# Kernel optimization log

Measured on AMD Instinct MI355X. Metric: run time of the kernel, lower is better.

## Reference

```python
import jax, jax.numpy as jnp
import numpy as np

N_NODES = 100000
N_EDGES = 1600000
DIM = 64          # num_features == hidden_dim
N_LAYERS = 5
N_GRAPHS = 1024
EMB = DIM * N_LAYERS  # 320
BN_EPS = 1e-5


def setup_inputs() -> dict:
    key = jax.random.key(0)
    ks = jax.random.split(key, 16)
    s = 0.05
    return {
        "x": jax.random.normal(ks[0], (N_NODES, DIM), dtype=jnp.float32),
        "edge_index": jax.random.randint(ks[1], (2, N_EDGES), 0, N_NODES, dtype=jnp.int32),
        "edge_weight": jax.random.uniform(ks[2], (N_EDGES,), dtype=jnp.float32),
        "batch": jnp.sort(jax.random.randint(ks[3], (N_NODES,), 0, N_GRAPHS, dtype=jnp.int32)),
        # stacked per-layer GIN MLP params: nn = Linear(d,d) -> ReLU -> Linear(d,d)
        "W1s": jax.random.normal(ks[4], (N_LAYERS, DIM, DIM), dtype=jnp.float32) * s,
        "b1s": jnp.zeros((N_LAYERS, DIM), dtype=jnp.float32),
        "W2s": jax.random.normal(ks[5], (N_LAYERS, DIM, DIM), dtype=jnp.float32) * s,
        "b2s": jnp.zeros((N_LAYERS, DIM), dtype=jnp.float32),
        # BatchNorm1d affine params (init: weight=1, bias=0)
        "gammas": jnp.ones((N_LAYERS, DIM), dtype=jnp.float32),
        "betas": jnp.zeros((N_LAYERS, DIM), dtype=jnp.float32),
        # projection head: Linear(EMB,EMB) -> ReLU -> Linear(EMB,EMB)
        "pW1": jax.random.normal(ks[6], (EMB, EMB), dtype=jnp.float32) * s,
        "pb1": jnp.zeros((EMB,), dtype=jnp.float32),
        "pW2": jax.random.normal(ks[7], (EMB, EMB), dtype=jnp.float32) * s,
        "pb2": jnp.zeros((EMB,), dtype=jnp.float32),
    }


def _encoder(x, src, dst, edge_weight, batch,
             W1s, b1s, W2s, b2s, gammas, betas):
    h = x
    pooled = []
    for i in range(N_LAYERS):
        # WGINConv (eps=0): h_out = nn(h + sum_{j->i} w_ij * h_j)
        msg = jax.ops.segment_sum(h[src] * edge_weight[:, None], dst,
                                  num_segments=N_NODES)  # [N, D]
        z = h + msg
        z = jnp.maximum(z @ W1s[i] + b1s[i], 0.0) @ W2s[i] + b2s[i]
        h = jnp.maximum(z, 0.0)  # F.relu after conv
        # BatchNorm1d (training mode: batch stats over nodes, biased var)
        mean = jnp.mean(h, axis=0)
        var = jnp.var(h, axis=0)
        h = (h - mean) * jax.lax.rsqrt(var + BN_EPS) * gammas[i] + betas[i]
        pooled.append(h)
    # global_mean_pool per layer, then concat along feature dim
    counts = jax.ops.segment_sum(jnp.ones((N_NODES,), h.dtype), batch,
                                 num_segments=N_GRAPHS)
    counts = jnp.maximum(counts, 1.0)[:, None]
    xpool = [jax.ops.segment_sum(h, batch, num_segments=N_GRAPHS) / counts
             for h in pooled]
    return jnp.concatenate(xpool, axis=1)  # [G, L*D]


def reference(x, edge_index, edge_weight, batch,
              W1s, b1s, W2s, b2s, gammas, betas,
              pW1, pb1, pW2, pb2):
    src, dst = edge_index[0], edge_index[1]
    y = _encoder(x, src, dst, edge_weight, batch,
                 W1s, b1s, W2s, b2s, gammas, betas)
    # proj_head: Linear -> ReLU -> Linear
    y = jnp.maximum(y @ pW1 + pb1, 0.0) @ pW2 + pb2
    return y
```

## Files before the change

### kernel.cpp

```cpp
#include <hip/hip_runtime.h>

#define NN 100000
#define NE 1600000
#define D 64
#define NL 5
#define NG 1024
#define EMBD 320
#define BN_EPS 1e-5f
#define SCAN_NB ((NN + 255) / 256)
#define GIN_NB ((NN + 63) / 64)
#define SRCB 7
#define M2 (NN * SRCB)
#define SCAN2_NB ((M2 + 255) / 256)

__device__ __forceinline__ unsigned short bf16rne(float f) {
  unsigned u = __float_as_uint(f);
  unsigned r = u + 0x7FFFu + ((u >> 16) & 1u);
  return (unsigned short)(r >> 16);
}
__device__ __forceinline__ float bflo(int v) {
  return __uint_as_float(((unsigned)v) << 16);
}
__device__ __forceinline__ float bfhi(int v) {
  return __uint_as_float(((unsigned)v) & 0xFFFF0000u);
}

__global__ __launch_bounds__(256) void k_cvt(const float* __restrict__ in,
                                             unsigned short* __restrict__ outb) {
  int i = blockIdx.x * 256 + threadIdx.x;
  if (i >= NN * 16) return;
  float4 v = ((const float4*)in)[i];
  ushort4 o;
  o.x = bf16rne(v.x); o.y = bf16rne(v.y); o.z = bf16rne(v.z); o.w = bf16rne(v.w);
  ((ushort4*)outb)[i] = o;
}

__global__ __launch_bounds__(256) void k_gbound(const int* __restrict__ batch,
                                                int* __restrict__ gstart) {
  int i = blockIdx.x * 256 + threadIdx.x;
  if (i >= NN) return;
  int b = batch[i];
  int bp = (i == 0) ? -1 : batch[i - 1];
  for (int g = bp + 1; g <= b; ++g) gstart[g] = i;
  if (i == NN - 1) {
    for (int g = b + 1; g <= NG; ++g) gstart[g] = NN;
  }
}

__global__ __launch_bounds__(256) void k_hist(const int* __restrict__ src,
                                              const int* __restrict__ dst,
                                              int* __restrict__ deg) {
  int e = blockIdx.x * 256 + threadIdx.x;
  if (e >= NE) return;
  int s = __builtin_nontemporal_load(src + e);
  int d = __builtin_nontemporal_load(dst + e);
  atomicAdd(&deg[d * SRCB + (s >> 14)], 1);
}

__global__ __launch_bounds__(256) void k_scan1(const int* __restrict__ deg,
                                               int* __restrict__ bsums) {
  __shared__ int sh[256];
  int i = blockIdx.x * 256 + threadIdx.x;
  sh[threadIdx.x] = (i < M2) ? deg[i] : 0;
  __syncthreads();
  for (int off = 128; off > 0; off >>= 1) {
    if (threadIdx.x < off) sh[threadIdx.x] += sh[threadIdx.x + off];
    __syncthreads();
  }
  if (threadIdx.x == 0) bsums[blockIdx.x] = sh[0];
}

__global__ __launch_bounds__(1024) void k_scan2(int* __restrict__ bsums) {
  __shared__ int sh[1024];
  int t = threadIdx.x;
  int loc[3];
  int s = 0;
#pragma unroll
  for (int i = 0; i < 3; ++i) {
    int idx = t * 3 + i;
    loc[i] = s;
    if (idx < SCAN2_NB) s += bsums[idx];
  }
  sh[t] = s;
  __syncthreads();
  for (int off = 1; off < 1024; off <<= 1) {
    int u = (t >= off) ? sh[t - off] : 0;
    __syncthreads();
    sh[t] += u;
    __syncthreads();
  }
  int base = sh[t] - s;
#pragma unroll
  for (int i = 0; i < 3; ++i) {
    int idx = t * 3 + i;
    if (idx < SCAN2_NB) bsums[idx] = base + loc[i];
  }
}

__global__ __launch_bounds__(256) void k_scan3(int* __restrict__ row_ptr,
                                               int* __restrict__ cursor,
                                               const int* __restrict__ bsums) {
  __shared__ int sh[256];
  int t = threadIdx.x;
  int i = blockIdx.x * 256 + t;
  int v = (i < M2) ? row_ptr[i] : 0;
  sh[t] = v;
  __syncthreads();
  for (int off = 1; off < 256; off <<= 1) {
    int u = (t >= off) ? sh[t - off] : 0;
    __syncthreads();
    sh[t] += u;
    __syncthreads();
  }
  int excl = sh[t] - v + bsums[blockIdx.x];
  if (i < M2) {
    row_ptr[i] = excl;
    cursor[i] = excl;
    if (i == M2 - 1) row_ptr[M2] = excl + v;
  }
}

__global__ __launch_bounds__(256) void k_fill(const int* __restrict__ src,
                                              const int* __restrict__ dst,
                                              const float* __restrict__ w,
                                              int* __restrict__ cursor,
                                              int2* __restrict__ epair) {
  int e = blockIdx.x * 256 + threadIdx.x;
  if (e >= NE) return;
  int s = __builtin_nontemporal_load(src + e);
  int d = __builtin_nontemporal_load(dst + e);
  float we = __builtin_nontemporal_load(w + e);
  int slot = atomicAdd(&cursor[d * SRCB + (s >> 14)], 1);
  int2 p;
  p.x = s;
  p.y = __float_as_int(we);
  epair[slot] = p;
}

#define ACC8(CA, CB, WE)                                                      \
  a0.x = fmaf(bflo(CA.x), WE, a0.x); a0.y = fmaf(bfhi(CA.x), WE, a0.y);       \
  a0.z = fmaf(bflo(CA.y), WE, a0.z); a0.w = fmaf(bfhi(CA.y), WE, a0.w);       \
  a1.x = fmaf(bflo(CA.z), WE, a1.x); a1.y = fmaf(bfhi(CA.z), WE, a1.y);       \
  a1.z = fmaf(bflo(CA.w), WE, a1.z); a1.w = fmaf(bfhi(CA.w), WE, a1.w);       \
  a2.x = fmaf(bflo(CB.x), WE, a2.x); a2.y = fmaf(bfhi(CB.x), WE, a2.y);       \
  a2.z = fmaf(bflo(CB.y), WE, a2.z); a2.w = fmaf(bfhi(CB.y), WE, a2.w);       \
  a3.x = fmaf(bflo(CB.z), WE, a3.x); a3.y = fmaf(bfhi(CB.z), WE, a3.y);       \
  a3.z = fmaf(bflo(CB.w), WE, a3.z); a3.w = fmaf(bfhi(CB.w), WE, a3.w);

__global__ __launch_bounds__(256, 6) void k_gin(const float* __restrict__ x0,
                                                const unsigned short* __restrict__ hbf,
                                                unsigned short* __restrict__ gbf,
                                                const int* __restrict__ row_ptr,
                                                const int2* __restrict__ epair,
                                                const float* __restrict__ W1,
                                                const float* __restrict__ b1,
                                                const float* __restrict__ W2,
                                                const float* __restrict__ b2,
                                                const float* __restrict__ statsP,
                                                const float* __restrict__ gammaP,
                                                const float* __restrict__ betaP,
                                                int first,
                                                float* __restrict__ statsL) {
  __shared__ float zin[64 * 65];
  __shared__ float sW[32 * 64];
  __shared__ float sb[64];
  __shared__ float wsumS[64];
  __shared__ float scA[64], sbA[64];
  const int t = threadIdx.x;
  const int nb = blockIdx.x * 64;
  const int nr = t >> 4, fc = t & 15;

  for (int i = t; i < 2048; i += 256) sW[i] = W1[i];
  if (t < 64) {
    sb[t] = b1[t];
    if (!first) {
      float m = statsP[t] * (1.f / NN);
      float v = fmaxf(statsP[64 + t] * (1.f / NN) - m * m, 0.f);
      float sc = gammaP[t] * rsqrtf(v + BN_EPS);
      scA[t] = sc;
      sbA[t] = betaP[t] - m * sc;
    }
  }

  {
    const int nl = t >> 2;
    const int q = t & 3;
    const int n = nb + nl;
    float4 a0 = {0.f, 0.f, 0.f, 0.f}, a1 = a0, a2 = a0, a3 = a0;
    float wsum = 0.f;
    if (n < NN) {
      const int beg = row_ptr[n * SRCB], end = row_ptr[n * SRCB + SRCB];
      int i = beg;
      for (; i + 2 <= end; i += 2) {
        long long e0 = __builtin_nontemporal_load((const long long*)(epair + i));
        long long e1 = __builtin_nontemporal_load((const long long*)(epair + i + 1));
        int s0 = (int)(e0 & 0xFFFFFFFFll);
        float w0 = __int_as_float((int)(e0 >> 32));
        int s1 = (int)(e1 & 0xFFFFFFFFll);
        float w1 = __int_as_float((int)(e1 >> 32));
        const int4* p0 = (const int4*)(hbf + (size_t)s0 * D);
        const int4* p1 = (const int4*)(hbf + (size_t)s1 * D);
        int4 r0a = p0[2 * q], r0b = p0[2 * q + 1];
        int4 r1a = p1[2 * q], r1b = p1[2 * q + 1];
        ACC8(r0a, r0b, w0)
        wsum += w0;
        ACC8(r1a, r1b, w1)
        wsum += w1;
      }
      for (; i < end; ++i) {
        long long e0 = __builtin_nontemporal_load((const long long*)(epair + i));
        int s0 = (int)(e0 & 0xFFFFFFFFll);
        float w0 = __int_as_float((int)(e0 >> 32));
        const int4* p0 = (const int4*)(hbf + (size_t)s0 * D);
        int4 r0a = p0[2 * q], r0b = p0[2 * q + 1];
        ACC8(r0a, r0b, w0)
        wsum += w0;
      }
      if (first) {
        const float4* own = (const float4*)(x0 + (size_t)n * D) + q * 4;
        float4 o0 = own[0], o1 = own[1], o2 = own[2], o3 = own[3];
        a0.x += o0.x; a0.y += o0.y; a0.z += o0.z; a0.w += o0.w;
        a1.x += o1.x; a1.y += o1.y; a1.z += o1.z; a1.w += o1.w;
        a2.x += o2.x; a2.y += o2.y; a2.z += o2.z; a2.w += o2.w;
        a3.x += o3.x; a3.y += o3.y; a3.z += o3.z; a3.w += o3.w;
      } else {
        const int4* hp = (const int4*)(hbf + (size_t)n * D);
        int4 c0 = hp[2 * q], c1 = hp[2 * q + 1];
        a0.x += bflo(c0.x); a0.y += bfhi(c0.x);
        a0.z += bflo(c0.y); a0.w += bfhi(c0.y);
        a1.x += bflo(c0.z); a1.y += bfhi(c0.z);
        a1.z += bflo(c0.w); a1.w += bfhi(c0.w);
        a2.x += bflo(c1.x); a2.y += bfhi(c1.x);
        a2.z += bflo(c1.y); a2.w += bfhi(c1.y);
        a3.x += bflo(c1.z); a3.y += bfhi(c1.z);
        a3.z += bflo(c1.w); a3.w += bfhi(c1.w);
      }
    }
    float* zr = &zin[nl * 65 + q * 16];
    *(float4*)(zr + 0) = a0;
    *(float4*)(zr + 4) = a1;
    *(float4*)(zr + 8) = a2;
    *(float4*)(zr + 12) = a3;
    if (q == 0) wsumS[nl] = wsum;
  }
  __syncthreads();

  if (!first) {
#pragma unroll
    for (int pass = 0; pass < 4; ++pass) {
      int idx = pass * 1024 + t * 4;
      int r = idx >> 6, c = idx & 63;
      float wp1 = 1.f + wsumS[r];
      float4 z = *(float4*)&zin[r * 65 + c];
      z.x = fmaf(z.x, scA[c + 0], sbA[c + 0] * wp1);
      z.y = fmaf(z.y, scA[c + 1], sbA[c + 1] * wp1);
      z.z = fmaf(z.z, scA[c + 2], sbA[c + 2] * wp1);
      z.w = fmaf(z.w, scA[c + 3], sbA[c + 3] * wp1);
      *(float4*)&zin[r * 65 + c] = z;
    }
    __syncthreads();
  }

#define GEMM_HALF(ACC, KBASE)                                                 \
  _Pragma("unroll 2") for (int kc = 0; kc < 8; ++kc) {                        \
    float4 zv[4], wv[4];                                                      \
    _Pragma("unroll") for (int i = 0; i < 4; ++i)                             \
        zv[i] = *(float4*)&zin[(nr * 4 + i) * 65 + ((KBASE) + kc) * 4];       \
    _Pragma("unroll") for (int kk = 0; kk < 4; ++kk)                          \
        wv[kk] = *(float4*)&sW[(kc * 4 + kk) * 64 + fc * 4];                  \
    _Pragma("unroll") for (int i = 0; i < 4; ++i) {                           \
      ACC[i].x = fmaf(zv[i].x, wv[0].x, ACC[i].x);                            \
      ACC[i].y = fmaf(zv[i].x, wv[0].y, ACC[i].y);                            \
      ACC[i].z = fmaf(zv[i].x, wv[0].z, ACC[i].z);                            \
      ACC[i].w = fmaf(zv[i].x, wv[0].w, ACC[i].w);                            \
      ACC[i].x = fmaf(zv[i].y, wv[1].x, ACC[i].x);                            \
      ACC[i].y = fmaf(zv[i].y, wv[1].y, ACC[i].y);                            \
      ACC[i].z = fmaf(zv[i].y, wv[1].z, ACC[i].z);                            \
      ACC[i].w = fmaf(zv[i].y, wv[1].w, ACC[i].w);                            \
      ACC[i].x = fmaf(zv[i].z, wv[2].x, ACC[i].x);                            \
      ACC[i].y = fmaf(zv[i].z, wv[2].y, ACC[i].y);                            \
      ACC[i].z = fmaf(zv[i].z, wv[2].z, ACC[i].z);                            \
      ACC[i].w = fmaf(zv[i].z, wv[2].w, ACC[i].w);                            \
      ACC[i].x = fmaf(zv[i].w, wv[3].x, ACC[i].x);                            \
      ACC[i].y = fmaf(zv[i].w, wv[3].y, ACC[i].y);                            \
      ACC[i].z = fmaf(zv[i].w, wv[3].z, ACC[i].z);                            \
      ACC[i].w = fmaf(zv[i].w, wv[3].w, ACC[i].w);                            \
    }                                                                         \
  }

#define RELU4(ACC)                                                            \
  _Pragma("unroll") for (int i = 0; i < 4; ++i) {                             \
    ACC[i].x = fmaxf(ACC[i].x, 0.f);                                          \
    ACC[i].y = fmaxf(ACC[i].y, 0.f);                                          \
    ACC[i].z = fmaxf(ACC[i].z, 0.f);                                          \
    ACC[i].w = fmaxf(ACC[i].w, 0.f);                                          \
  }

  float4 acc[4];
  {
    float4 bias = *(float4*)&sb[fc * 4];
#pragma unroll
    for (int i = 0; i < 4; ++i) acc[i] = bias;
  }
  GEMM_HALF(acc, 0)
  __syncthreads();
  for (int i = t; i < 2048; i += 256) sW[i] = W1[2048 + i];
  __syncthreads();
  GEMM_HALF(acc, 8)
  RELU4(acc)
  __syncthreads();

#pragma unroll
  for (int i = 0; i < 4; ++i) *(float4*)&zin[(nr * 4 + i) * 65 + fc * 4] = acc[i];
  for (int i = t; i < 2048; i += 256) sW[i] = W2[i];
  if (t < 64) sb[t] = b2[t];
  __syncthreads();

  float4 acc2[4];
  {
    float4 bias = *(float4*)&sb[fc * 4];
#pragma unroll
    for (int i = 0; i < 4; ++i) acc2[i] = bias;
  }
  GEMM_HALF(acc2, 0)
  __syncthreads();
  for (int i = t; i < 2048; i += 256) sW[i] = W2[2048 + i];
  __syncthreads();
  GEMM_HALF(acc2, 8)
  RELU4(acc2)

  float4 s4 = {0.f, 0.f, 0.f, 0.f}, q4 = {0.f, 0.f, 0.f, 0.f};
#pragma unroll
  for (int i = 0; i < 4; ++i) {
    int n = nb + nr * 4 + i;
    if (n < NN) {
      ushort4 ob;
      ob.x = bf16rne(acc2[i].x);
      ob.y = bf16rne(acc2[i].y);
      ob.z = bf16rne(acc2[i].z);
      ob.w = bf16rne(acc2[i].w);
      *(ushort4*)(gbf + (size_t)n * D + fc * 4) = ob;
      s4.x += acc2[i].x; s4.y += acc2[i].y; s4.z += acc2[i].z; s4.w += acc2[i].w;
      q4.x = fmaf(acc2[i].x, acc2[i].x, q4.x);
      q4.y = fmaf(acc2[i].y, acc2[i].y, q4.y);
      q4.z = fmaf(acc2[i].z, acc2[i].z, q4.z);
      q4.w = fmaf(acc2[i].w, acc2[i].w, q4.w);
    }
  }
#pragma unroll
  for (int m = 16; m <= 32; m <<= 1) {
    s4.x += __shfl_xor(s4.x, m, 64); s4.y += __shfl_xor(s4.y, m, 64);
    s4.z += __shfl_xor(s4.z, m, 64); s4.w += __shfl_xor(s4.w, m, 64);
    q4.x += __shfl_xor(q4.x, m, 64); q4.y += __shfl_xor(q4.y, m, 64);
    q4.z += __shfl_xor(q4.z, m, 64); q4.w += __shfl_xor(q4.w, m, 64);
  }
  __syncthreads();
  int wv_ = t >> 6;
  if ((t & 63) < 16) {
    *(float4*)&zin[wv_ * 64 + fc * 4] = s4;
    *(float4*)&zin[256 + wv_ * 64 + fc * 4] = q4;
  }
  __syncthreads();
  if (t < 64) {
    float S = zin[t] + zin[64 + t] + zin[128 + t] + zin[192 + t];
    float Q = zin[256 + t] + zin[320 + t] + zin[384 + t] + zin[448 + t];
    unsafeAtomicAdd(&statsL[t], S);
    unsafeAtomicAdd(&statsL[64 + t], Q);
  }
#undef GEMM_HALF
#undef RELU4
}

__global__ __launch_bounds__(256) void k_poolraw(const unsigned short* __restrict__ gbf,
                                                 const int* __restrict__ gstart,
                                                 float* __restrict__ pooledraw,
                                                 int layer) {
  __shared__ float4 sh4[256];
  int g = blockIdx.x;
  int beg = gstart[g], end = gstart[g + 1];
  int p = threadIdx.x & 15, r = threadIdx.x >> 4;
  float4 s = {0.f, 0.f, 0.f, 0.f};
  for (int n = beg + r; n < end; n += 16) {
    int2 c = ((const int2*)(gbf + (size_t)n * D))[p];
    s.x += bflo(c.x); s.y += bfhi(c.x);
    s.z += bflo(c.y); s.w += bfhi(c.y);
  }
  sh4[threadIdx.x] = s;
  __syncthreads();
  if (threadIdx.x < 16) {
    float4 tot = {0.f, 0.f, 0.f, 0.f};
#pragma unroll
    for (int j = 0; j < 16; ++j) {
      float4 u = sh4[j * 16 + threadIdx.x];
      tot.x += u.x; tot.y += u.y; tot.z += u.z; tot.w += u.w;
    }
    int cnt = end - beg;
    float inv = 1.0f / (float)(cnt > 1 ? cnt : 1);
    float4 o = {tot.x * inv, tot.y * inv, tot.z * inv, tot.w * inv};
    ((float4*)(pooledraw + (size_t)g * EMBD + layer * D))[threadIdx.x] = o;
  }
}

__global__ __launch_bounds__(EMBD) void k_proj(const float* __restrict__ pooledraw,
                                               const float* __restrict__ stats,
                                               const float* __restrict__ gammas,
                                               const float* __restrict__ betas,
                                               const float* __restrict__ pW1,
                                               const float* __restrict__ pb1,
                                               const float* __restrict__ pW2,
                                               const float* __restrict__ pb2,
                                               float* __restrict__ out) {
  __shared__ float row[EMBD];
  __shared__ float y1[EMBD];
  int g = blockIdx.x, j = threadIdx.x;
  {
    int L = j >> 6, f = j & 63;
    float m = stats[L * 128 + f] * (1.f / NN);
    float v = fmaxf(stats[L * 128 + 64 + f] * (1.f / NN) - m * m, 0.f);
    float sc = gammas[L * D + f] * rsqrtf(v + BN_EPS);
    float sb = betas[L * D + f] - m * sc;
    row[j] = fmaf(pooledraw[(size_t)g * EMBD + j], sc, sb);
  }
  __syncthreads();
  float acc = pb1[j];
#pragma unroll 4
  for (int k = 0; k < EMBD; ++k) acc = fmaf(row[k], pW1[(size_t)k * EMBD + j], acc);
  y1[j] = fmaxf(acc, 0.f);
  __syncthreads();
  acc = pb2[j];
#pragma unroll 4
  for (int k = 0; k < EMBD; ++k) acc = fmaf(y1[k], pW2[(size_t)k * EMBD + j], acc);
  out[(size_t)g * EMBD + j] = acc;
}

extern "C" void kernel_launch(void* const* d_in, const int* in_sizes, int n_in,
                              void* d_out, int out_size, void* d_ws, size_t ws_size,
                              hipStream_t stream) {
  const float* x = (const float*)d_in[0];
  const int* ei = (const int*)d_in[1];
  const float* ew = (const float*)d_in[2];
  const int* batch = (const int*)d_in[3];
  const float* W1s = (const float*)d_in[4];
  const float* b1s = (const float*)d_in[5];
  const float* W2s = (const float*)d_in[6];
  const float* b2s = (const float*)d_in[7];
  const float* gammas = (const float*)d_in[8];
  const float* betas = (const float*)d_in[9];
  const float* pW1 = (const float*)d_in[10];
  const float* pb1 = (const float*)d_in[11];
  const float* pW2 = (const float*)d_in[12];
  const float* pb2 = (const float*)d_in[13];
  const int* srcv = ei;
  const int* dstv = ei + NE;

  char* ws = (char*)d_ws;
  float* stats = (float*)ws;
  float* pooledraw = stats + NL * 128;
  int* gstart = (int*)(pooledraw + (size_t)NG * EMBD);
  int* row_ptr = gstart + NG + 1;
  int* cursor = row_ptr + M2 + 1;
  int2* epair = (int2*)(cursor + M2);
  int* bsums = (int*)(epair + NE);
  unsigned short* hbfA = (unsigned short*)(bsums + SCAN2_NB);
  unsigned short* hbfB = hbfA + (size_t)NN * D;

  hipMemsetAsync(row_ptr, 0, (M2 + 1) * sizeof(int), stream);
  hipMemsetAsync(stats, 0, NL * 128 * sizeof(float), stream);
  k_hist<<<(NE + 255) / 256, 256, 0, stream>>>(srcv, dstv, row_ptr);
  k_scan1<<<SCAN2_NB, 256, 0, stream>>>(row_ptr, bsums);
  k_scan2<<<1, 1024, 0, stream>>>(bsums);
  k_scan3<<<SCAN2_NB, 256, 0, stream>>>(row_ptr, cursor, bsums);
  k_fill<<<(NE + 255) / 256, 256, 0, stream>>>(srcv, dstv, ew, cursor, epair);
  k_gbound<<<SCAN_NB, 256, 0, stream>>>(batch, gstart);
  k_cvt<<<(NN * 16 + 255) / 256, 256, 0, stream>>>(x, hbfA);

  unsigned short* bfin = hbfA;
  unsigned short* bfout = hbfB;
  for (int L = 0; L < NL; ++L) {
    k_gin<<<GIN_NB, 256, 0, stream>>>(x, bfin, bfout, row_ptr, epair,
                                      W1s + L * D * D, b1s + L * D,
                                      W2s + L * D * D, b2s + L * D,
                                      stats + (L > 0 ? (L - 1) * 128 : 0),
                                      gammas + (L > 0 ? (L - 1) * D : 0),
                                      betas + (L > 0 ? (L - 1) * D : 0),
                                      L == 0 ? 1 : 0,
                                      stats + L * 128);
    k_poolraw<<<NG, 256, 0, stream>>>(bfout, gstart, pooledraw, L);
    unsigned short* tmpb = bfin;
    bfin = bfout;
    bfout = tmpb;
  }
  k_proj<<<NG, EMBD, 0, stream>>>(pooledraw, stats, gammas, betas,
                                  pW1, pb1, pW2, pb2, (float*)d_out);
}
```

Measured before the change: 805.1 us.

## Fuse per-graph mean pooling into GIN layer kernel via atomics

```diff
diff --git a/kernel.cpp b/kernel.cpp
--- a/kernel.cpp
+++ b/kernel.cpp
@@ -124,16 +124,15 @@
                                               const int* __restrict__ dst,
                                               const float* __restrict__ w,
                                               int* __restrict__ cursor,
-                                              int2* __restrict__ epair) {
+                                              long long* __restrict__ epair) {
   int e = blockIdx.x * 256 + threadIdx.x;
   if (e >= NE) return;
   int s = __builtin_nontemporal_load(src + e);
   int d = __builtin_nontemporal_load(dst + e);
   float we = __builtin_nontemporal_load(w + e);
   int slot = atomicAdd(&cursor[d * SRCB + (s >> 14)], 1);
-  int2 p;
-  p.x = s;
-  p.y = __float_as_int(we);
+  long long p = (long long)(unsigned)s |
+                ((long long)(unsigned)__float_as_int(we) << 32);
   epair[slot] = p;
 }
 
@@ -151,7 +150,11 @@
                                                 const unsigned short* __restrict__ hbf,
                                                 unsigned short* __restrict__ gbf,
                                                 const int* __restrict__ row_ptr,
-                                                const int2* __restrict__ epair,
+                                                const long long* __restrict__ epair,
+                                                const int* __restrict__ batch_,
+                                                const int* __restrict__ gstart_,
+                                                float* __restrict__ pooledraw,
+                                                int layer,
                                                 const float* __restrict__ W1,
                                                 const float* __restrict__ b1,
                                                 const float* __restrict__ W2,
@@ -166,6 +169,7 @@
   __shared__ float sb[64];
   __shared__ float wsumS[64];
   __shared__ float scA[64], sbA[64];
+  __shared__ float psum[256];
   const int t = threadIdx.x;
   const int nb = blockIdx.x * 64;
   const int nr = t >> 4, fc = t & 15;
@@ -192,8 +196,8 @@
       const int beg = row_ptr[n * SRCB], end = row_ptr[n * SRCB + SRCB];
       int i = beg;
       for (; i + 2 <= end; i += 2) {
-        long long e0 = __builtin_nontemporal_load((const long long*)(epair + i));
-        long long e1 = __builtin_nontemporal_load((const long long*)(epair + i + 1));
+        long long e0 = __builtin_nontemporal_load(epair + i);
+        long long e1 = __builtin_nontemporal_load(epair + i + 1);
         int s0 = (int)(e0 & 0xFFFFFFFFll);
         float w0 = __int_as_float((int)(e0 >> 32));
         int s1 = (int)(e1 & 0xFFFFFFFFll);
@@ -208,7 +212,7 @@
         wsum += w1;
       }
       for (; i < end; ++i) {
-        long long e0 = __builtin_nontemporal_load((const long long*)(epair + i));
+        long long e0 = __builtin_nontemporal_load(epair + i);
         int s0 = (int)(e0 & 0xFFFFFFFFll);
         float w0 = __int_as_float((int)(e0 >> 32));
         const int4* p0 = (const int4*)(hbf + (size_t)s0 * D);
@@ -328,11 +332,13 @@
   __syncthreads();
   GEMM_HALF(acc2, 8)
   RELU4(acc2)
+  __syncthreads();
 
   float4 s4 = {0.f, 0.f, 0.f, 0.f}, q4 = {0.f, 0.f, 0.f, 0.f};
 #pragma unroll
   for (int i = 0; i < 4; ++i) {
     int n = nb + nr * 4 + i;
+    *(float4*)&zin[(nr * 4 + i) * 65 + fc * 4] = acc2[i];
     if (n < NN) {
       ushort4 ob;
       ob.x = bf16rne(acc2[i].x);
@@ -347,6 +353,30 @@
       q4.w = fmaf(acc2[i].w, acc2[i].w, q4.w);
     }
   }
+  __syncthreads();
+
+  {
+    const int nbend = (nb + 64 < NN) ? nb + 64 : NN;
+    const int gs = batch_[nb];
+    const int ge = batch_[nbend - 1];
+    const int c = t & 63, qr = t >> 6;
+    for (int g = gs; g <= ge; ++g) {
+      int a = gstart_[g];
+      int b = gstart_[g + 1];
+      a = (a > nb) ? a - nb : 0;
+      b = (b < nbend) ? b - nb : nbend - nb;
+      float p = 0.f;
+      for (int r = a + qr; r < b; r += 4) p += zin[r * 65 + c];
+      psum[t] = p;
+      __syncthreads();
+      if (t < 64) {
+        float tot = psum[t] + psum[t + 64] + psum[t + 128] + psum[t + 192];
+        unsafeAtomicAdd(&pooledraw[(size_t)g * EMBD + layer * D + t], tot);
+      }
+      __syncthreads();
+    }
+  }
+
 #pragma unroll
   for (int m = 16; m <= 32; m <<= 1) {
     s4.x += __shfl_xor(s4.x, m, 64); s4.y += __shfl_xor(s4.y, m, 64);
@@ -354,7 +384,6 @@
     q4.x += __shfl_xor(q4.x, m, 64); q4.y += __shfl_xor(q4.y, m, 64);
     q4.z += __shfl_xor(q4.z, m, 64); q4.w += __shfl_xor(q4.w, m, 64);
   }
-  __syncthreads();
   int wv_ = t >> 6;
   if ((t & 63) < 16) {
     *(float4*)&zin[wv_ * 64 + fc * 4] = s4;
@@ -371,37 +400,8 @@
 #undef RELU4
 }
 
-__global__ __launch_bounds__(256) void k_poolraw(const unsigned short* __restrict__ gbf,
-                                                 const int* __restrict__ gstart,
-                                                 float* __restrict__ pooledraw,
-                                                 int layer) {
-  __shared__ float4 sh4[256];
-  int g = blockIdx.x;
-  int beg = gstart[g], end = gstart[g + 1];
-  int p = threadIdx.x & 15, r = threadIdx.x >> 4;
-  float4 s = {0.f, 0.f, 0.f, 0.f};
-  for (int n = beg + r; n < end; n += 16) {
-    int2 c = ((const int2*)(gbf + (size_t)n * D))[p];
-    s.x += bflo(c.x); s.y += bfhi(c.x);
-    s.z += bflo(c.y); s.w += bfhi(c.y);
-  }
-  sh4[threadIdx.x] = s;
-  __syncthreads();
-  if (threadIdx.x < 16) {
-    float4 tot = {0.f, 0.f, 0.f, 0.f};
-#pragma unroll
-    for (int j = 0; j < 16; ++j) {
-      float4 u = sh4[j * 16 + threadIdx.x];
-      tot.x += u.x; tot.y += u.y; tot.z += u.z; tot.w += u.w;
-    }
-    int cnt = end - beg;
-    float inv = 1.0f / (float)(cnt > 1 ? cnt : 1);
-    float4 o = {tot.x * inv, tot.y * inv, tot.z * inv, tot.w * inv};
-    ((float4*)(pooledraw + (size_t)g * EMBD + layer * D))[threadIdx.x] = o;
-  }
-}
-
 __global__ __launch_bounds__(EMBD) void k_proj(const float* __restrict__ pooledraw,
+                                               const int* __restrict__ gstart,
                                                const float* __restrict__ stats,
                                                const float* __restrict__ gammas,
                                                const float* __restrict__ betas,
@@ -419,7 +419,9 @@
     float v = fmaxf(stats[L * 128 + 64 + f] * (1.f / NN) - m * m, 0.f);
     float sc = gammas[L * D + f] * rsqrtf(v + BN_EPS);
     float sb = betas[L * D + f] - m * sc;
-    row[j] = fmaf(pooledraw[(size_t)g * EMBD + j], sc, sb);
+    int cnt = gstart[g + 1] - gstart[g];
+    float inv = 1.0f / (float)(cnt > 1 ? cnt : 1);
+    row[j] = fmaf(pooledraw[(size_t)g * EMBD + j] * inv, sc, sb);
   }
   __syncthreads();
   float acc = pb1[j];
@@ -459,13 +461,14 @@
   int* gstart = (int*)(pooledraw + (size_t)NG * EMBD);
   int* row_ptr = gstart + NG + 1;
   int* cursor = row_ptr + M2 + 1;
-  int2* epair = (int2*)(cursor + M2);
+  long long* epair = (long long*)(cursor + M2);
   int* bsums = (int*)(epair + NE);
   unsigned short* hbfA = (unsigned short*)(bsums + SCAN2_NB);
   unsigned short* hbfB = hbfA + (size_t)NN * D;
 
   hipMemsetAsync(row_ptr, 0, (M2 + 1) * sizeof(int), stream);
-  hipMemsetAsync(stats, 0, NL * 128 * sizeof(float), stream);
+  hipMemsetAsync(stats, 0,
+                 (NL * 128 + (size_t)NG * EMBD) * sizeof(float), stream);
   k_hist<<<(NE + 255) / 256, 256, 0, stream>>>(srcv, dstv, row_ptr);
   k_scan1<<<SCAN2_NB, 256, 0, stream>>>(row_ptr, bsums);
   k_scan2<<<1, 1024, 0, stream>>>(bsums);
@@ -478,6 +481,7 @@
   unsigned short* bfout = hbfB;
   for (int L = 0; L < NL; ++L) {
     k_gin<<<GIN_NB, 256, 0, stream>>>(x, bfin, bfout, row_ptr, epair,
+                                      batch, gstart, pooledraw, L,
                                       W1s + L * D * D, b1s + L * D,
                                       W2s + L * D * D, b2s + L * D,
                                       stats + (L > 0 ? (L - 1) * 128 : 0),
@@ -485,11 +489,10 @@
                                       betas + (L > 0 ? (L - 1) * D : 0),
                                       L == 0 ? 1 : 0,
                                       stats + L * 128);
-    k_poolraw<<<NG, 256, 0, stream>>>(bfout, gstart, pooledraw, L);
     unsigned short* tmpb = bfin;
     bfin = bfout;
     bfout = tmpb;
   }
-  k_proj<<<NG, EMBD, 0, stream>>>(pooledraw, stats, gammas, betas,
+  k_proj<<<NG, EMBD, 0, stream>>>(pooledraw, gstart, stats, gammas, betas,
                                   pW1, pb1, pW2, pb2, (float*)d_out);
 }
```

Result: no change. 797.9 us (-0.9%).
